# Kernel tuning notes

Hardware: AMD Instinct MI355X
Metric: run time of the kernel (lower is better)

The kernel has to match this reference:

```python
import jax, jax.numpy as jnp
import numpy as np

D_MODEL, D_FF, N_EXPERTS, TOP_K = 1024, 2048, 8, 2
B, S = 2, 2048

def setup_inputs() -> dict:
    key = jax.random.key(0)
    k1, k2, k3, k4 = jax.random.split(key, 4)
    scale = 0.02
    return {
        "x": jax.random.normal(k1, (B, S, D_MODEL), dtype=jnp.float32),
        "gate_w": jax.random.normal(k2, (D_MODEL, N_EXPERTS), dtype=jnp.float32) * scale,
        "w1": jax.random.normal(k3, (N_EXPERTS, D_MODEL, D_FF), dtype=jnp.float32) * scale,
        "w2": jax.random.normal(k4, (N_EXPERTS, D_FF, D_MODEL), dtype=jnp.float32) * scale,
    }

def reference(x, gate_w, w1, w2):
    # --- Router (eval mode: no exploration noise, no dropout) ---
    router_logits = jnp.einsum('bsd,de->bse', x, gate_w)          # [B,S,E]
    top_logits, top_idx = jax.lax.top_k(router_logits, TOP_K)      # [B,S,K]
    top_w = jax.nn.softmax(top_logits, axis=-1)                    # [B,S,K]
    # topk indices are distinct per token, so per-(token,expert) combine weight
    # is the sum over k of weight_k * 1[idx_k == e] (matches torch gather/argmax logic)
    combine = jnp.sum(
        jax.nn.one_hot(top_idx, N_EXPERTS, dtype=x.dtype) * top_w[..., None],
        axis=-2)                                                   # [B,S,E]
    # --- Experts: dense-compute formulation of the gather/MLP/scatter loop ---
    h = jax.nn.silu(jnp.einsum('bsd,edf->ebsf', x, w1))            # [E,B,S,Dff]
    y = jnp.einsum('ebsf,efd->ebsd', h, w2)                        # [E,B,S,D]
    out = jnp.einsum('ebsd,bse->bsd', y, combine)                  # [B,S,D]
    return out
```

## Files before the change

### kernel.cpp

```cpp
#include <hip/hip_runtime.h>
#include <cstdint>
#include <cstddef>

#define D_MODEL 1024
#define D_FF    2048
#define N_EXP   8
#define NTOK    4096
#define NASSIGN (NTOK * 2)
#define MAXTILE 72

typedef __bf16 bf16_t;
typedef bf16_t bf16x8 __attribute__((ext_vector_type(8)));
typedef float  f32x4  __attribute__((ext_vector_type(4)));

typedef __attribute__((address_space(3))) void       lds_void;
typedef const __attribute__((address_space(1))) void gl_void;

__device__ __forceinline__ unsigned short f2b(float f) {
  union { float f; unsigned u; } v; v.f = f;
  unsigned u = v.u;
  unsigned r = (u + 0x7FFFu + ((u >> 16) & 1u)) >> 16;
  return (unsigned short)r;
}
__device__ __forceinline__ float b2f(unsigned short b) {
  union { unsigned u; float f; } v; v.u = ((unsigned)b) << 16; return v.f;
}

__device__ __forceinline__ void transpose_pair(
    const float* __restrict__ ein, unsigned short* __restrict__ eout,
    int R, int C, int c00, int r0, unsigned* T0, unsigned* T1, int tid)
{
  const int g = tid >> 4;
  const int m = tid & 15;
  const int sh = (g & 1) * 16;

  float4 v[2][4];
  #pragma unroll
  for (int t = 0; t < 2; ++t)
    #pragma unroll
    for (int i = 0; i < 4; ++i)
      v[t][i] = *(const float4*)(ein + (size_t)(r0 + i * 16 + g) * C + (c00 + t * 64) + m * 4);

  #pragma unroll
  for (int i = 0; i < 4; ++i) {
    unsigned lo = (unsigned)f2b(v[0][i].x) | ((unsigned)f2b(v[0][i].y) << 16);
    unsigned hi = (unsigned)f2b(v[0][i].z) | ((unsigned)f2b(v[0][i].w) << 16);
    unsigned* p = T0 + (i * 16 + g) * 33 + m * 2;
    p[0] = lo; p[1] = hi;
  }
  __syncthreads();
  #pragma unroll
  for (int i = 0; i < 4; ++i) {
    unsigned lo = (unsigned)f2b(v[1][i].x) | ((unsigned)f2b(v[1][i].y) << 16);
    unsigned hi = (unsigned)f2b(v[1][i].z) | ((unsigned)f2b(v[1][i].w) << 16);
    unsigned* p = T1 + (i * 16 + g) * 33 + m * 2;
    p[0] = lo; p[1] = hi;
  }
  #pragma unroll
  for (int i = 0; i < 4; ++i) {
    int c = i * 16 + g;
    ushort4 o;
    o.x = (unsigned short)(T0[(4 * m + 0) * 33 + (c >> 1)] >> sh);
    o.y = (unsigned short)(T0[(4 * m + 1) * 33 + (c >> 1)] >> sh);
    o.z = (unsigned short)(T0[(4 * m + 2) * 33 + (c >> 1)] >> sh);
    o.w = (unsigned short)(T0[(4 * m + 3) * 33 + (c >> 1)] >> sh);
    *(ushort4*)(eout + (size_t)(c00 + c) * R + r0 + m * 4) = o;
  }
  __syncthreads();
  #pragma unroll
  for (int i = 0; i < 4; ++i) {
    int c = i * 16 + g;
    ushort4 o;
    o.x = (unsigned short)(T1[(4 * m + 0) * 33 + (c >> 1)] >> sh);
    o.y = (unsigned short)(T1[(4 * m + 1) * 33 + (c >> 1)] >> sh);
    o.z = (unsigned short)(T1[(4 * m + 2) * 33 + (c >> 1)] >> sh);
    o.w = (unsigned short)(T1[(4 * m + 3) * 33 + (c >> 1)] >> sh);
    *(ushort4*)(eout + (size_t)(c00 + c + 64) * R + r0 + m * 4) = o;
  }
}

__global__ __launch_bounds__(256) void prep_k(
    const float* __restrict__ x, const float* __restrict__ gw,
    const float* __restrict__ w1, const float* __restrict__ w2,
    unsigned short* __restrict__ w1t, unsigned short* __restrict__ w2t,
    int* __restrict__ eidx, float* __restrict__ ewt)
{
  __shared__ unsigned T[2][64 * 33];
  const int bid = blockIdx.x;
  const int tid = threadIdx.x;

  if (bid < 2048) {
    int e = bid >> 8, rem = bid & 255;
    int bx2 = rem & 15, by = rem >> 4;
    transpose_pair(w1 + (size_t)e * D_MODEL * D_FF,
                   w1t + (size_t)e * D_MODEL * D_FF,
                   D_MODEL, D_FF, bx2 * 128, by * 64, T[0], T[1], tid);
    return;
  }
  if (bid < 4096) {
    int b = bid - 2048;
    int e = b >> 8, rem = b & 255;
    int bx2 = rem & 7, by = rem >> 3;
    transpose_pair(w2 + (size_t)e * D_MODEL * D_FF,
                   w2t + (size_t)e * D_MODEL * D_FF,
                   D_FF, D_MODEL, bx2 * 128, by * 64, T[0], T[1], tid);
    return;
  }
  const int rb = bid - 4096;
  const int wv = tid >> 6, lane = tid & 63;
  const int token = rb * 4 + wv;
  const float4* xr4 = (const float4*)(x + (size_t)token * D_MODEL);
  const float4* gw4 = (const float4*)gw;

  float acc[8] = {};
  #pragma unroll
  for (int it = 0; it < 4; ++it) {
    float4 xv = xr4[it * 64 + lane];
    int d0 = it * 256 + lane * 4;
    #pragma unroll
    for (int i = 0; i < 4; ++i) {
      int d = d0 + i;
      float4 g0 = gw4[d * 2];
      float4 g1 = gw4[d * 2 + 1];
      float xs = (i == 0) ? xv.x : (i == 1) ? xv.y : (i == 2) ? xv.z : xv.w;
      acc[0] += xs * g0.x; acc[1] += xs * g0.y;
      acc[2] += xs * g0.z; acc[3] += xs * g0.w;
      acc[4] += xs * g1.x; acc[5] += xs * g1.y;
      acc[6] += xs * g1.z; acc[7] += xs * g1.w;
    }
  }
  #pragma unroll
  for (int m = 1; m < 64; m <<= 1) {
    #pragma unroll
    for (int k = 0; k < 8; ++k) acc[k] += __shfl_xor(acc[k], m);
  }
  if (lane == 0) {
    int i1 = 0; float v1 = acc[0];
    #pragma unroll
    for (int k = 1; k < 8; ++k) if (acc[k] > v1) { v1 = acc[k]; i1 = k; }
    int i2 = -1; float v2 = -1e30f;
    #pragma unroll
    for (int k = 0; k < 8; ++k) if (k != i1 && acc[k] > v2) { v2 = acc[k]; i2 = k; }
    float t  = __expf(v2 - v1);
    float wa = 1.f / (1.f + t);
    float wb = t * wa;
    eidx[token * 2 + 0] = i1; eidx[token * 2 + 1] = i2;
    ewt [token * 2 + 0] = wa; ewt [token * 2 + 1] = wb;
  }
}

__global__ __launch_bounds__(1024) void scan_k(
    const int* __restrict__ eidx, const float* __restrict__ ewt,
    int* __restrict__ counts, int* __restrict__ offsets,
    int* __restrict__ rowtok, float* __restrict__ rowwt, int* __restrict__ rowof,
    int* __restrict__ tile_e, int* __restrict__ tile_m0, int* __restrict__ tile_n)
{
  __shared__ int wtot[16][9];
  __shared__ int woff[16][9];
  __shared__ int soff[8];
  const int t = threadIdx.x, w = t >> 6, lane = t & 63;

  int4 a = ((const int4*)eidx)[t * 2];
  int4 b = ((const int4*)eidx)[t * 2 + 1];
  int my[8] = {a.x, a.y, a.z, a.w, b.x, b.y, b.z, b.w};
  int pre[8], local[8] = {};
  #pragma unroll
  for (int i = 0; i < 8; ++i) { pre[i] = local[my[i]]; local[my[i]]++; }

  int inc[8];
  #pragma unroll
  for (int e = 0; e < 8; ++e) inc[e] = local[e];
  #pragma unroll
  for (int d = 1; d < 64; d <<= 1) {
    #pragma unroll
    for (int e = 0; e < 8; ++e) {
      int v = __shfl_up(inc[e], d);
      if (lane >= d) inc[e] += v;
    }
  }
  if (lane == 63) {
    #pragma unroll
    for (int e = 0; e < 8; ++e) wtot[w][e] = inc[e];
  }
  __syncthreads();

  if (t < 8) {
    int e = t, run = 0;
    #pragma unroll
    for (int ww = 0; ww < 16; ++ww) { woff[ww][e] = run; run += wtot[ww][e]; }
    wtot[0][e] = run;
  }
  __syncthreads();

  if (t == 0) {
    int o = 0, tt = 0;
    for (int e = 0; e < 8; ++e) {
      int c = wtot[0][e];
      counts[e] = c;
      offsets[e] = o;
      soff[e] = o;
      int nt = (c + 127) >> 7;
      for (int i = 0; i < nt; ++i) { tile_e[tt] = e; tile_m0[tt] = i * 128; ++tt; }
      o += c;
    }
    tile_n[0] = tt;
  }
  __syncthreads();

  int base_[8];
  #pragma unroll
  for (int e = 0; e < 8; ++e) base_[e] = soff[e] + woff[w][e] + inc[e] - local[e];

  float4 wa4 = ((const float4*)ewt)[t * 2];
  float4 wb4 = ((const float4*)ewt)[t * 2 + 1];
  float wv[8] = {wa4.x, wa4.y, wa4.z, wa4.w, wb4.x, wb4.y, wb4.z, wb4.w};

  #pragma unroll
  for (int i = 0; i < 8; ++i) {
    int bb = t * 8 + i, e = my[i];
    int row = base_[e] + pre[i];
    rowtok[row] = bb >> 1;
    rowwt[row]  = wv[i];
    rowof[bb]   = row;
  }
}

__global__ __launch_bounds__(256) void gather_k(
    const float* __restrict__ x, const int* __restrict__ rowtok,
    unsigned short* __restrict__ Xe)
{
  const int row = blockIdx.x;
  const int token = rowtok[row];
  const float4* xr = (const float4*)(x + (size_t)token * D_MODEL);
  ushort4* dst = (ushort4*)(Xe + (size_t)row * D_MODEL);
  float4 v = xr[threadIdx.x];
  ushort4 o;
  o.x = f2b(v.x); o.y = f2b(v.y); o.z = f2b(v.z); o.w = f2b(v.w);
  dst[threadIdx.x] = o;
}

template<int K, int N, int NT_LOG2, int MODE>
__global__ __launch_bounds__(256) void moe_gemm_k(
    const unsigned short* __restrict__ A,
    const unsigned short* __restrict__ Bt,
    unsigned short* __restrict__ Hout,
    const int* __restrict__ counts, const int* __restrict__ offsets,
    const float* __restrict__ rowwt,
    const int* __restrict__ tile_e, const int* __restrict__ tile_m0,
    const int* __restrict__ tile_n)
{
  const int t = blockIdx.x >> NT_LOG2;
  if (t >= tile_n[0]) return;
  const int e   = tile_e[t];
  const int m0  = tile_m0[t];
  const int n0  = (blockIdx.x & ((1 << NT_LOG2) - 1)) * 128;
  const int cnt = counts[e];
  const int base = offsets[e];

  __shared__ unsigned short lA[128 * 32];
  __shared__ unsigned short lB[128 * 32];

  const int tid = threadIdx.x;
  const int lane = tid & 63;
  const int wv = tid >> 6;
  const int wm = wv & 1, wn = wv >> 1;
  const int col = lane & 15, quad = lane >> 4;

  const unsigned short* Aseg = A + (size_t)base * K;
  const unsigned short* Bseg = Bt + (size_t)e * ((size_t)N * K);

  const int lrow = lane >> 2;
  const int gch  = (lane & 3) ^ ((lane >> 2) & 3) ^ ((lane >> 4) & 3);
  const int fsw  = (col & 3) ^ ((col >> 2) & 3);

  f32x4 acc[4][4] = {};

  for (int k0 = 0; k0 < K; k0 += 32) {
    __syncthreads();
    #pragma unroll
    for (int r = 0; r < 2; ++r) {
      int s = r * 4 + wv;
      int row = s * 16 + lrow;
      const char* gA = (const char*)Aseg + ((size_t)(m0 + row) * K + k0) * 2 + gch * 16;
      const char* gB = (const char*)Bseg + ((size_t)(n0 + row) * K + k0) * 2 + gch * 16;
      __builtin_amdgcn_global_load_lds((gl_void*)gA, (lds_void*)((char*)lA + s * 1024), 16, 0, 0);
      __builtin_amdgcn_global_load_lds((gl_void*)gB, (lds_void*)((char*)lB + s * 1024), 16, 0, 0);
    }
    __syncthreads();

    bf16x8 af[4], bfr[4];
    #pragma unroll
    for (int i = 0; i < 4; ++i) {
      int r = wm * 64 + i * 16 + col;
      int p = quad ^ fsw;
      af[i] = *(const bf16x8*)(lA + r * 32 + p * 8);
    }
    #pragma unroll
    for (int j = 0; j < 4; ++j) {
      int r = wn * 64 + j * 16 + col;
      int p = quad ^ fsw;
      bfr[j] = *(const bf16x8*)(lB + r * 32 + p * 8);
    }
    #pragma unroll
    for (int i = 0; i < 4; ++i)
      #pragma unroll
      for (int j = 0; j < 4; ++j)
        acc[i][j] = __builtin_amdgcn_mfma_f32_16x16x32_bf16(af[i], bfr[j], acc[i][j], 0, 0, 0);
  }

  #pragma unroll
  for (int i = 0; i < 4; ++i) {
    #pragma unroll
    for (int reg = 0; reg < 4; ++reg) {
      int r = m0 + wm * 64 + i * 16 + quad * 4 + reg;
      if (r < cnt) {
        unsigned short* hrow = Hout + (size_t)(base + r) * N + (n0 + wn * 64 + col);
        if (MODE == 1) {
          #pragma unroll
          for (int j = 0; j < 4; ++j) {
            float v = acc[i][j][reg];
            float s = v / (1.f + __expf(-v));
            hrow[j * 16] = f2b(s);
          }
        } else {
          float wgt = rowwt[base + r];
          #pragma unroll
          for (int j = 0; j < 4; ++j)
            hrow[j * 16] = f2b(wgt * acc[i][j][reg]);
        }
      }
    }
  }
}

__global__ __launch_bounds__(256) void combine_k(
    const unsigned short* __restrict__ Y, const int* __restrict__ rowof,
    float* __restrict__ out)
{
  const int token = blockIdx.x;
  const int r1 = rowof[token * 2];
  const int r2 = rowof[token * 2 + 1];
  const int d4 = threadIdx.x;
  ushort4 a = *(const ushort4*)(Y + (size_t)r1 * D_MODEL + d4 * 4);
  ushort4 b = *(const ushort4*)(Y + (size_t)r2 * D_MODEL + d4 * 4);
  float4 o;
  o.x = b2f(a.x) + b2f(b.x);
  o.y = b2f(a.y) + b2f(b.y);
  o.z = b2f(a.z) + b2f(b.z);
  o.w = b2f(a.w) + b2f(b.w);
  *(float4*)(out + (size_t)token * D_MODEL + d4 * 4) = o;
}

extern "C" void kernel_launch(void* const* d_in, const int* in_sizes, int n_in,
                              void* d_out, int out_size, void* d_ws, size_t ws_size,
                              hipStream_t stream) {
  const float* x  = (const float*)d_in[0];
  const float* gw = (const float*)d_in[1];
  const float* w1 = (const float*)d_in[2];
  const float* w2 = (const float*)d_in[3];
  float* out = (float*)d_out;

  char* ws = (char*)d_ws;
  size_t off = 0;
  auto alloc = [&](size_t bytes) -> char* {
    char* p = ws + off; off += (bytes + 255) & ~(size_t)255; return p;
  };
  int*   ctrl    = (int*)alloc(1024);
  int*   counts  = ctrl;
  int*   offsets = ctrl + 8;
  int*   tile_n  = ctrl + 16;
  int*   tile_e  = ctrl + 32;
  int*   tile_m0 = ctrl + 32 + MAXTILE;
  int*   eidx    = (int*)  alloc((size_t)NASSIGN * 4);
  float* ewt     = (float*)alloc((size_t)NASSIGN * 4);
  int*   rowtok  = (int*)  alloc((size_t)NASSIGN * 4);
  float* rowwt   = (float*)alloc((size_t)NASSIGN * 4);
  int*   rowof   = (int*)  alloc((size_t)NASSIGN * 4);
  unsigned short* Xe  = (unsigned short*)alloc((size_t)(NASSIGN + 128) * D_MODEL * 2);
  unsigned short* H   = (unsigned short*)alloc((size_t)(NASSIGN + 128) * D_FF * 2);
  unsigned short* Y   = (unsigned short*)alloc((size_t)(NASSIGN + 128) * D_MODEL * 2);
  unsigned short* w1t = (unsigned short*)alloc((size_t)N_EXP * D_MODEL * D_FF * 2);
  unsigned short* w2t = (unsigned short*)alloc((size_t)N_EXP * D_MODEL * D_FF * 2);

  prep_k<<<4096 + NTOK / 4, 256, 0, stream>>>(x, gw, w1, w2, w1t, w2t, eidx, ewt);
  scan_k<<<1, 1024, 0, stream>>>(eidx, ewt, counts, offsets, rowtok, rowwt, rowof,
                                 tile_e, tile_m0, tile_n);
  gather_k<<<NASSIGN, 256, 0, stream>>>(x, rowtok, Xe);

  moe_gemm_k<D_MODEL, D_FF, 4, 1><<<MAXTILE * 16, 256, 0, stream>>>(
      Xe, w1t, H, counts, offsets, rowwt, tile_e, tile_m0, tile_n);
  moe_gemm_k<D_FF, D_MODEL, 3, 2><<<MAXTILE * 8, 256, 0, stream>>>(
      H, w2t, Y, counts, offsets, rowwt, tile_e, tile_m0, tile_n);
  combine_k<<<NTOK, 256, 0, stream>>>(Y, rowof, out);
}
```

Baseline: 346.4 us.

## Widen weight transpose strips and remap GEMM blocks for XCD-aware tile ordering

The weight transpose-and-convert in prep_k now handles four 64-column sub-tiles per block instead of two, ping-ponging between two LDS buffers, which halves the number of transpose blocks. In the MoE GEMMs, blocks are remapped so that blockIdx mod 8 selects a contiguous chunk of work items, ordered N-tile-major, so that blocks sharing an XCD share the same weight columns. Only valid work items are enumerated, so fewer blocks exit early. The changes add register pressure from 16 float4 loads per thread and an integer division per block.

```diff
diff --git a/kernel.cpp b/kernel.cpp
--- a/kernel.cpp
+++ b/kernel.cpp
@@ -26,7 +26,7 @@
   union { unsigned u; float f; } v; v.u = ((unsigned)b) << 16; return v.f;
 }
 
-__device__ __forceinline__ void transpose_pair(
+__device__ __forceinline__ void transpose_strip4(
     const float* __restrict__ ein, unsigned short* __restrict__ eout,
     int R, int C, int c00, int r0, unsigned* T0, unsigned* T1, int tid)
 {
@@ -34,49 +34,44 @@
   const int m = tid & 15;
   const int sh = (g & 1) * 16;
 
-  float4 v[2][4];
-  #pragma unroll
-  for (int t = 0; t < 2; ++t)
+  float4 v[4][4];
+  #pragma unroll
+  for (int t = 0; t < 4; ++t)
     #pragma unroll
     for (int i = 0; i < 4; ++i)
       v[t][i] = *(const float4*)(ein + (size_t)(r0 + i * 16 + g) * C + (c00 + t * 64) + m * 4);
 
-  #pragma unroll
-  for (int i = 0; i < 4; ++i) {
-    unsigned lo = (unsigned)f2b(v[0][i].x) | ((unsigned)f2b(v[0][i].y) << 16);
-    unsigned hi = (unsigned)f2b(v[0][i].z) | ((unsigned)f2b(v[0][i].w) << 16);
-    unsigned* p = T0 + (i * 16 + g) * 33 + m * 2;
-    p[0] = lo; p[1] = hi;
-  }
-  __syncthreads();
-  #pragma unroll
-  for (int i = 0; i < 4; ++i) {
-    unsigned lo = (unsigned)f2b(v[1][i].x) | ((unsigned)f2b(v[1][i].y) << 16);
-    unsigned hi = (unsigned)f2b(v[1][i].z) | ((unsigned)f2b(v[1][i].w) << 16);
-    unsigned* p = T1 + (i * 16 + g) * 33 + m * 2;
-    p[0] = lo; p[1] = hi;
-  }
-  #pragma unroll
-  for (int i = 0; i < 4; ++i) {
-    int c = i * 16 + g;
-    ushort4 o;
-    o.x = (unsigned short)(T0[(4 * m + 0) * 33 + (c >> 1)] >> sh);
-    o.y = (unsigned short)(T0[(4 * m + 1) * 33 + (c >> 1)] >> sh);
-    o.z = (unsigned short)(T0[(4 * m + 2) * 33 + (c >> 1)] >> sh);
-    o.w = (unsigned short)(T0[(4 * m + 3) * 33 + (c >> 1)] >> sh);
-    *(ushort4*)(eout + (size_t)(c00 + c) * R + r0 + m * 4) = o;
-  }
-  __syncthreads();
-  #pragma unroll
-  for (int i = 0; i < 4; ++i) {
-    int c = i * 16 + g;
-    ushort4 o;
-    o.x = (unsigned short)(T1[(4 * m + 0) * 33 + (c >> 1)] >> sh);
-    o.y = (unsigned short)(T1[(4 * m + 1) * 33 + (c >> 1)] >> sh);
-    o.z = (unsigned short)(T1[(4 * m + 2) * 33 + (c >> 1)] >> sh);
-    o.w = (unsigned short)(T1[(4 * m + 3) * 33 + (c >> 1)] >> sh);
-    *(ushort4*)(eout + (size_t)(c00 + c + 64) * R + r0 + m * 4) = o;
-  }
+  #define PACK(BUF, VT)                                                      \
+    _Pragma("unroll")                                                        \
+    for (int i = 0; i < 4; ++i) {                                            \
+      unsigned lo = (unsigned)f2b(VT[i].x) | ((unsigned)f2b(VT[i].y) << 16); \
+      unsigned hi = (unsigned)f2b(VT[i].z) | ((unsigned)f2b(VT[i].w) << 16); \
+      unsigned* p = (BUF) + (i * 16 + g) * 33 + m * 2;                       \
+      p[0] = lo; p[1] = hi;                                                  \
+    }
+  #define STORE(BUF, T)                                                      \
+    _Pragma("unroll")                                                        \
+    for (int i = 0; i < 4; ++i) {                                            \
+      int c = i * 16 + g;                                                    \
+      ushort4 o;                                                             \
+      o.x = (unsigned short)((BUF)[(4 * m + 0) * 33 + (c >> 1)] >> sh);      \
+      o.y = (unsigned short)((BUF)[(4 * m + 1) * 33 + (c >> 1)] >> sh);      \
+      o.z = (unsigned short)((BUF)[(4 * m + 2) * 33 + (c >> 1)] >> sh);      \
+      o.w = (unsigned short)((BUF)[(4 * m + 3) * 33 + (c >> 1)] >> sh);      \
+      *(ushort4*)(eout + (size_t)(c00 + (T) * 64 + c) * R + r0 + m * 4) = o; \
+    }
+
+  PACK(T0, v[0]);
+  __syncthreads();
+  STORE(T0, 0); PACK(T1, v[1]);
+  __syncthreads();
+  STORE(T1, 1); PACK(T0, v[2]);
+  __syncthreads();
+  STORE(T0, 2); PACK(T1, v[3]);
+  __syncthreads();
+  STORE(T1, 3);
+  #undef PACK
+  #undef STORE
 }
 
 __global__ __launch_bounds__(256) void prep_k(
@@ -89,24 +84,24 @@
   const int bid = blockIdx.x;
   const int tid = threadIdx.x;
 
+  if (bid < 1024) {
+    int e = bid >> 7, rem = bid & 127;
+    int bs = rem & 7, by = rem >> 3;
+    transpose_strip4(w1 + (size_t)e * D_MODEL * D_FF,
+                     w1t + (size_t)e * D_MODEL * D_FF,
+                     D_MODEL, D_FF, bs * 256, by * 64, T[0], T[1], tid);
+    return;
+  }
   if (bid < 2048) {
-    int e = bid >> 8, rem = bid & 255;
-    int bx2 = rem & 15, by = rem >> 4;
-    transpose_pair(w1 + (size_t)e * D_MODEL * D_FF,
-                   w1t + (size_t)e * D_MODEL * D_FF,
-                   D_MODEL, D_FF, bx2 * 128, by * 64, T[0], T[1], tid);
+    int b = bid - 1024;
+    int e = b >> 7, rem = b & 127;
+    int bs = rem & 3, by = rem >> 2;
+    transpose_strip4(w2 + (size_t)e * D_MODEL * D_FF,
+                     w2t + (size_t)e * D_MODEL * D_FF,
+                     D_FF, D_MODEL, bs * 256, by * 64, T[0], T[1], tid);
     return;
   }
-  if (bid < 4096) {
-    int b = bid - 2048;
-    int e = b >> 8, rem = b & 255;
-    int bx2 = rem & 7, by = rem >> 3;
-    transpose_pair(w2 + (size_t)e * D_MODEL * D_FF,
-                   w2t + (size_t)e * D_MODEL * D_FF,
-                   D_FF, D_MODEL, bx2 * 128, by * 64, T[0], T[1], tid);
-    return;
-  }
-  const int rb = bid - 4096;
+  const int rb = bid - 2048;
   const int wv = tid >> 6, lane = tid & 63;
   const int token = rb * 4 + wv;
   const float4* xr4 = (const float4*)(x + (size_t)token * D_MODEL);
@@ -249,11 +244,16 @@
     const int* __restrict__ tile_e, const int* __restrict__ tile_m0,
     const int* __restrict__ tile_n)
 {
-  const int t = blockIdx.x >> NT_LOG2;
-  if (t >= tile_n[0]) return;
+  const int nm = tile_n[0];
+  const int nitems = nm << NT_LOG2;
+  const int per = (nitems + 7) >> 3;
+  const int w = (blockIdx.x & 7) * per + (blockIdx.x >> 3);
+  if (w >= nitems) return;
+  const int nidx = w / nm;
+  const int t = w - nidx * nm;
   const int e   = tile_e[t];
   const int m0  = tile_m0[t];
-  const int n0  = (blockIdx.x & ((1 << NT_LOG2) - 1)) * 128;
+  const int n0  = nidx * 128;
   const int cnt = counts[e];
   const int base = offsets[e];
 
@@ -382,7 +382,7 @@
   unsigned short* w1t = (unsigned short*)alloc((size_t)N_EXP * D_MODEL * D_FF * 2);
   unsigned short* w2t = (unsigned short*)alloc((size_t)N_EXP * D_MODEL * D_FF * 2);
 
-  prep_k<<<4096 + NTOK / 4, 256, 0, stream>>>(x, gw, w1, w2, w1t, w2t, eidx, ewt);
+  prep_k<<<2048 + NTOK / 4, 256, 0, stream>>>(x, gw, w1, w2, w1t, w2t, eidx, ewt);
   scan_k<<<1, 1024, 0, stream>>>(eidx, ewt, counts, offsets, rowtok, rowwt, rowof,
                                  tile_e, tile_m0, tile_n);
   gather_k<<<NASSIGN, 256, 0, stream>>>(x, rowtok, Xe);
```

Result: no change. 351.0 us (+1.3%).
